# Kernel optimization log

Hardware: AMD Instinct MI355X
Metric: run time of the kernel (lower is better)

The kernel has to match this reference:

```python
import jax, jax.numpy as jnp
import numpy as np

N_NODES = 50000
N_EDGES = 800000
D_IN = 128
HID = [128, 64, 64]
N_CLASSES = 2
N_PROTO = 8
K = N_CLASSES * N_PROTO  # 16 = mlp_input_dim


def setup_inputs() -> dict:
    key = jax.random.key(0)
    ks = jax.random.split(key, 16)
    def lin(k, fi, fo):
        kw, kb = jax.random.split(k)
        s = 1.0 / np.sqrt(fi)
        return (jax.random.uniform(kw, (fi, fo), jnp.float32, -s, s),
                jax.random.uniform(kb, (fo,), jnp.float32, -s, s))
    W1, b1 = lin(ks[0], D_IN, HID[0])
    W2, b2 = lin(ks[1], HID[0], HID[1])
    W3, b3 = lin(ks[2], HID[1], HID[2])
    Wf0, bf0 = lin(ks[3], K, K // 2)
    Wf1, bf1 = lin(ks[4], K // 2, 1)
    return {
        'x': jax.random.normal(ks[5], (N_NODES, D_IN), jnp.float32),
        'edge_index': jax.random.randint(ks[6], (2, N_EDGES), 0, N_NODES, jnp.int64),
        'y': jax.random.randint(ks[7], (N_NODES,), 0, 2, jnp.int64),
        'W1': W1, 'b1': b1, 'W2': W2, 'b2': b2, 'W3': W3, 'b3': b3,
        'prototypes': jax.random.normal(ks[8], (N_CLASSES, N_PROTO, HID[2]), jnp.float32),
        'Wf0': Wf0, 'bf0': bf0, 'Wf1': Wf1, 'bf1': bf1,
    }


def reference(x, edge_index, y, W1, b1, W2, b2, W3, b3, prototypes, Wf0, bf0, Wf1, bf1):
    n = x.shape[0]
    loop = jnp.arange(n, dtype=edge_index.dtype)
    src = jnp.concatenate([edge_index[0], loop])  # A + I self loops (GCNConv default)
    dst = jnp.concatenate([edge_index[1], loop])
    deg = jax.ops.segment_sum(jnp.ones(src.shape[0], x.dtype), dst, num_segments=n)
    dinv = jax.lax.rsqrt(deg)  # deg >= 1 thanks to self loops
    enorm = dinv[src] * dinv[dst]  # sym-normalized edge weights

    def gcn(h, W, b):
        msg = (h @ W)[src] * enorm[:, None]  # gather + transform
        return jax.ops.segment_sum(msg, dst, num_segments=n) + b  # scatter-add

    h = jax.nn.relu(gcn(x, W1, b1))
    h = jax.nn.relu(gcn(h, W2, b2))
    h = jax.nn.relu(gcn(h, W3, b3))  # [n, 64]

    prot = prototypes.reshape(-1, prototypes.shape[-1])  # [K, 64]
    d2 = jnp.maximum(jnp.sum(h * h, -1, keepdims=True)
                     + jnp.sum(prot * prot, -1)[None, :]
                     - 2.0 * (h @ prot.T), 0.0)  # squared Euclidean [n, K]
    sim = jnp.log((d2 + 1.0) / (d2 + 1e-4))

    # MLPReadout, eval mode (dropout inactive), exact GELU like torch nn.GELU
    z = jax.nn.gelu(sim @ Wf0 + bf0, approximate=False)
    out = jax.nn.sigmoid(z @ Wf1 + bf1)
    return (out.squeeze(), y.astype(jnp.float32))
```

## Files before the change

kernel.cpp:

```cpp
#include <hip/hip_runtime.h>
#include <hip/hip_bf16.h>
#include <math.h>


typedef __attribute__((ext_vector_type(8))) short short8;
typedef __attribute__((ext_vector_type(4))) float f32x4;

#define BKT_SHIFT 5
#define BKT_NODES 32
#define EPB 2048
#define LCAP 1024
#define PREPN 28672
#define PREPB 112

__device__ __forceinline__ short f2bs(float x) {
    __hip_bfloat16 b = __float2bfloat16(x);
    return *reinterpret_cast<short*>(&b);
}
__device__ __forceinline__ float2 bpair(unsigned u) {
    float lo = __uint_as_float(u << 16);
    float hi = __uint_as_float(u & 0xffff0000u);
    return make_float2(lo, hi);
}
__device__ __forceinline__ unsigned packbf(float a, float b) {
    unsigned la = (unsigned)(unsigned short)f2bs(a);
    unsigned hb = (unsigned)(unsigned short)f2bs(b);
    return la | (hb << 16);
}

__device__ __forceinline__ void block_excl_scan(int* __restrict__ arr, int n, int t) {
    __shared__ int wsums[4];
    int lane = t & 63, wv = t >> 6;
    int carry = 0;
    for (int c0 = 0; c0 < n; c0 += 256) {
        int i = c0 + t;
        int v = (i < n) ? arr[i] : 0;
        int orig = v;
#pragma unroll
        for (int off = 1; off < 64; off <<= 1) {
            int u = __shfl_up(v, off, 64);
            if (lane >= off) v += u;
        }
        if (lane == 63) wsums[wv] = v;
        __syncthreads();
        int w0 = wsums[0], w1 = wsums[1], w2 = wsums[2], w3 = wsums[3];
        int woff = (wv > 0 ? w0 : 0) + (wv > 1 ? w1 : 0) + (wv > 2 ? w2 : 0);
        int tot = w0 + w1 + w2 + w3;
        __syncthreads();
        if (i < n) arr[i] = carry + woff + (v - orig);
        carry += tot;
    }
}


__global__ __launch_bounds__(256) void sort_local_kernel(const int* __restrict__ ei, int E,
                                                         int NB, int B,
                                                         int* __restrict__ glens,
                                                         int* __restrict__ gstart,
                                                         int* __restrict__ edge_sorted,
                                                         const float* __restrict__ W1,
                                                         const float* __restrict__ W2,
                                                         const float* __restrict__ W3,
                                                         __hip_bfloat16* __restrict__ Wp1,
                                                         __hip_bfloat16* __restrict__ Wp2,
                                                         __hip_bfloat16* __restrict__ Wp3) {
    int t = threadIdx.x;
    if ((int)blockIdx.x >= B) {
        int i = ((int)blockIdx.x - B) * 256 + t;
        if (i < 16384) {
            int k = i >> 7, n = i & 127;
            Wp1[(((k >> 3) * 128) + n) * 8 + (k & 7)] = __float2bfloat16(W1[i]);
        } else if (i < 24576) {
            int j = i - 16384;
            int k = j >> 6, n = j & 63;
            Wp2[(((k >> 3) * 64) + n) * 8 + (k & 7)] = __float2bfloat16(W2[j]);
        } else if (i < PREPN) {
            int j = i - 24576;
            int k = j >> 6, n = j & 63;
            Wp3[(((k >> 3) * 64) + n) * 8 + (k & 7)] = __float2bfloat16(W3[j]);
        }
        return;
    }
    extern __shared__ int lds[];
    int* hist  = lds;
    int* lbase = lds + NB;
    int* sortd = lds + 2 * NB;
    int blk = blockIdx.x;
    int e0 = blk * EPB;
    int cnt = E - e0;
    if (cnt > EPB) cnt = EPB;

    for (int i = t; i < NB; i += 256) hist[i] = 0;
    __syncthreads();
    for (int i = t; i < cnt; i += 256) {
        int dst = ei[E + e0 + i];
        atomicAdd(&hist[dst >> BKT_SHIFT], 1);
    }
    __syncthreads();
    for (int i = t; i < NB; i += 256) lbase[i] = hist[i];
    __syncthreads();
    block_excl_scan(lbase, NB, t);
    __syncthreads();
    for (int i = t; i < NB; i += 256) {
        glens[(size_t)blk * NB + i] = hist[i];
        gstart[(size_t)blk * NB + i] = lbase[i];
    }
    __syncthreads();
    for (int i = t; i < cnt; i += 256) {
        int src = ei[e0 + i];
        int dst = ei[E + e0 + i];
        int pos = atomicAdd(&lbase[dst >> BKT_SHIFT], 1);
        sortd[pos] = (src << BKT_SHIFT) | (dst & (BKT_NODES - 1));
    }
    __syncthreads();
    for (int i = t; i < cnt; i += 256) edge_sorted[e0 + i] = sortd[i];
}

__global__ __launch_bounds__(256) void csr_build_kernel(const int* __restrict__ edge_sorted,
                                                        const int* __restrict__ glens,
                                                        const int* __restrict__ gstart,
                                                        int NB, int B, int N,
                                                        int* __restrict__ row_beg,
                                                        int* __restrict__ row_end,
                                                        float* __restrict__ dinv,
                                                        int* __restrict__ csr) {
    __shared__ int lruns[512];
    __shared__ int loffs[512];
    __shared__ int sdeg[BKT_NODES];
    __shared__ int scur[BKT_NODES];
    __shared__ int raw[LCAP];
    __shared__ int srt[LCAP];
    int b = blockIdx.x;
    int t = threadIdx.x;

    for (int i = t; i < 512; i += 256) {
        int v = (i < B) ? glens[(size_t)i * NB + b] : 0;
        lruns[i] = v;
        loffs[i] = v;
    }
    if (t < BKT_NODES) sdeg[t] = 0;
    __syncthreads();
    block_excl_scan(loffs, B, t);
    __syncthreads();
    int cnt = loffs[B - 1] + lruns[B - 1];
    if (cnt > LCAP) cnt = LCAP;

    for (int r = t; r < B; r += 256) {
        int len = lruns[r];
        if (len) {
            int off = loffs[r];
            int st = r * EPB + gstart[(size_t)r * NB + b];
            for (int k = 0; k < len; ++k) {
                int p = off + k;
                if (p < LCAP) raw[p] = edge_sorted[st + k];
            }
        }
    }
    __syncthreads();

    for (int i = t; i < cnt; i += 256) atomicAdd(&sdeg[raw[i] & (BKT_NODES - 1)], 1);
    __syncthreads();
    int base = b * LCAP;
    if (t < BKT_NODES) {
        int ssum = 0;
        for (int i = 0; i < t; ++i) ssum += sdeg[i];
        scur[t] = ssum;
        int node = b * BKT_NODES + t;
        if (node < N) {
            row_beg[node] = base + ssum;
            row_end[node] = base + ssum + sdeg[t];
            dinv[node] = rsqrtf((float)(sdeg[t] + 1));
        }
    }
    __syncthreads();
    for (int i = t; i < cnt; i += 256) {
        int p = raw[i];
        int pos = atomicAdd(&scur[p & (BKT_NODES - 1)], 1);
        srt[pos] = p >> BKT_SHIFT;
    }
    __syncthreads();
    for (int i = t; i < cnt; i += 256) csr[base + i] = srt[i];
}


template <int DI, int DO, bool AF32>
__global__ __launch_bounds__(256) void mfma_gemm_kernel(const void* __restrict__ Av,
                                                        const __hip_bfloat16* __restrict__ Wp,
                                                        const float* __restrict__ dinv,
                                                        __hip_bfloat16* __restrict__ C, int N) {
    constexpr int NT = DO / 16;
    int t = threadIdx.x;
    int wave = t >> 6, lane = t & 63;
    int q = lane >> 4, l16 = lane & 15;
    int rbase = blockIdx.x * 64 + wave * 16;
    int row = rbase + l16;
    int rowc = row < N ? row : N - 1;

    f32x4 acc[NT];
#pragma unroll
    for (int i = 0; i < NT; ++i) acc[i] = (f32x4){0.f, 0.f, 0.f, 0.f};

#pragma unroll
    for (int kt = 0; kt < DI / 32; ++kt) {
        int k0 = kt * 32 + q * 8;
        short8 afrag;
        if (AF32) {
            const float* A = (const float*)Av;
            const float* ap = A + (size_t)rowc * DI + k0;
            float4 lo = *(const float4*)ap;
            float4 hi = *(const float4*)(ap + 4);
            afrag[0] = f2bs(lo.x); afrag[1] = f2bs(lo.y);
            afrag[2] = f2bs(lo.z); afrag[3] = f2bs(lo.w);
            afrag[4] = f2bs(hi.x); afrag[5] = f2bs(hi.y);
            afrag[6] = f2bs(hi.z); afrag[7] = f2bs(hi.w);
        } else {
            const __hip_bfloat16* A = (const __hip_bfloat16*)Av;
            afrag = *(const short8*)(A + (size_t)rowc * DI + k0);
        }
        const short8* wrow = (const short8*)(Wp + (size_t)(kt * 4 + q) * DO * 8);
#pragma unroll
        for (int tt = 0; tt < NT; ++tt) {
            short8 bfrag = wrow[tt * 16 + l16];
            acc[tt] = __builtin_amdgcn_mfma_f32_16x16x32_bf16(afrag, bfrag, acc[tt], 0, 0, 0);
        }
    }
#pragma unroll
    for (int r = 0; r < 4; ++r) {
        int gr = rbase + q * 4 + r;
        if (gr < N) {
            float dv = dinv[gr];
#pragma unroll
            for (int tt = 0; tt < NT; ++tt)
                C[(size_t)gr * DO + tt * 16 + l16] = __float2bfloat16(acc[tt][r] * dv);
        }
    }
}


__global__ __launch_bounds__(256) void agg128_kernel(const uint4* __restrict__ tmp,
                                                     const float* __restrict__ bias,
                                                     const float* __restrict__ dinv,
                                                     const int* __restrict__ row_beg,
                                                     const int* __restrict__ row_end,
                                                     const int* __restrict__ csr_src,
                                                     uint4* __restrict__ outp, int N) {
    int lane = threadIdx.x & 63;
    int q = lane >> 4, sub = lane & 15;
    int node = blockIdx.x * 4 + (threadIdx.x >> 6);
    if (node >= N) return;
    float dvi = dinv[node];
    float a0 = 0, a1 = 0, a2 = 0, a3 = 0, a4 = 0, a5 = 0, a6 = 0, a7 = 0;
    if (q == 0) {
        uint4 sv = tmp[(size_t)node * 16 + sub];
        float2 p0 = bpair(sv.x), p1 = bpair(sv.y), p2 = bpair(sv.z), p3 = bpair(sv.w);
        a0 = p0.x; a1 = p0.y; a2 = p1.x; a3 = p1.y;
        a4 = p2.x; a5 = p2.y; a6 = p3.x; a7 = p3.y;
    }
    int beg = row_beg[node], end = row_end[node];
    for (int j = beg; j < end; j += 64) {
        int m = end - j;
        if (m > 64) m = 64;
        int s = (lane < m) ? csr_src[j + lane] : 0;
        int iters = (m + 3) >> 2;
        for (int k = 0; k < iters; ++k) {
            int e = 4 * k + q;
            int ec = (e < m) ? e : 0;
            int sk = __shfl(s, ec, 64);
            uint4 v = tmp[(size_t)sk * 16 + sub];
            if (e < m) {
                float2 p0 = bpair(v.x), p1 = bpair(v.y), p2 = bpair(v.z), p3 = bpair(v.w);
                a0 += p0.x; a1 += p0.y; a2 += p1.x; a3 += p1.y;
                a4 += p2.x; a5 += p2.y; a6 += p3.x; a7 += p3.y;
            }
        }
    }
    a0 += __shfl_xor(a0, 16, 64); a1 += __shfl_xor(a1, 16, 64);
    a2 += __shfl_xor(a2, 16, 64); a3 += __shfl_xor(a3, 16, 64);
    a4 += __shfl_xor(a4, 16, 64); a5 += __shfl_xor(a5, 16, 64);
    a6 += __shfl_xor(a6, 16, 64); a7 += __shfl_xor(a7, 16, 64);
    a0 += __shfl_xor(a0, 32, 64); a1 += __shfl_xor(a1, 32, 64);
    a2 += __shfl_xor(a2, 32, 64); a3 += __shfl_xor(a3, 32, 64);
    a4 += __shfl_xor(a4, 32, 64); a5 += __shfl_xor(a5, 32, 64);
    a6 += __shfl_xor(a6, 32, 64); a7 += __shfl_xor(a7, 32, 64);
    if (q == 0) {
        float4 b0 = *(const float4*)&bias[sub * 8];
        float4 b1 = *(const float4*)&bias[sub * 8 + 4];
        uint4 o;
        o.x = packbf(fmaxf(dvi * a0 + b0.x, 0.f), fmaxf(dvi * a1 + b0.y, 0.f));
        o.y = packbf(fmaxf(dvi * a2 + b0.z, 0.f), fmaxf(dvi * a3 + b0.w, 0.f));
        o.z = packbf(fmaxf(dvi * a4 + b1.x, 0.f), fmaxf(dvi * a5 + b1.y, 0.f));
        o.w = packbf(fmaxf(dvi * a6 + b1.z, 0.f), fmaxf(dvi * a7 + b1.w, 0.f));
        outp[(size_t)node * 16 + sub] = o;
    }
}

__global__ __launch_bounds__(256) void agg64_kernel(const uint4* __restrict__ tmp,
                                                    const float* __restrict__ bias,
                                                    const float* __restrict__ dinv,
                                                    const int* __restrict__ row_beg,
                                                    const int* __restrict__ row_end,
                                                    const int* __restrict__ csr_src,
                                                    uint4* __restrict__ outp, int N) {
    int lane = threadIdx.x & 63;
    int o8 = lane >> 3, sub = lane & 7;
    int node = blockIdx.x * 4 + (threadIdx.x >> 6);
    if (node >= N) return;
    float dvi = dinv[node];
    float a0 = 0, a1 = 0, a2 = 0, a3 = 0, a4 = 0, a5 = 0, a6 = 0, a7 = 0;
    if (o8 == 0) {
        uint4 sv = tmp[(size_t)node * 8 + sub];
        float2 p0 = bpair(sv.x), p1 = bpair(sv.y), p2 = bpair(sv.z), p3 = bpair(sv.w);
        a0 = p0.x; a1 = p0.y; a2 = p1.x; a3 = p1.y;
        a4 = p2.x; a5 = p2.y; a6 = p3.x; a7 = p3.y;
    }
    int beg = row_beg[node], end = row_end[node];
    for (int j = beg; j < end; j += 64) {
        int m = end - j;
        if (m > 64) m = 64;
        int s = (lane < m) ? csr_src[j + lane] : 0;
        int iters = (m + 7) >> 3;
        for (int k = 0; k < iters; ++k) {
            int e = 8 * k + o8;
            int ec = (e < m) ? e : 0;
            int sk = __shfl(s, ec, 64);
            uint4 v = tmp[(size_t)sk * 8 + sub];
            if (e < m) {
                float2 p0 = bpair(v.x), p1 = bpair(v.y), p2 = bpair(v.z), p3 = bpair(v.w);
                a0 += p0.x; a1 += p0.y; a2 += p1.x; a3 += p1.y;
                a4 += p2.x; a5 += p2.y; a6 += p3.x; a7 += p3.y;
            }
        }
    }
    a0 += __shfl_xor(a0, 8, 64); a1 += __shfl_xor(a1, 8, 64);
    a2 += __shfl_xor(a2, 8, 64); a3 += __shfl_xor(a3, 8, 64);
    a4 += __shfl_xor(a4, 8, 64); a5 += __shfl_xor(a5, 8, 64);
    a6 += __shfl_xor(a6, 8, 64); a7 += __shfl_xor(a7, 8, 64);
    a0 += __shfl_xor(a0, 16, 64); a1 += __shfl_xor(a1, 16, 64);
    a2 += __shfl_xor(a2, 16, 64); a3 += __shfl_xor(a3, 16, 64);
    a4 += __shfl_xor(a4, 16, 64); a5 += __shfl_xor(a5, 16, 64);
    a6 += __shfl_xor(a6, 16, 64); a7 += __shfl_xor(a7, 16, 64);
    a0 += __shfl_xor(a0, 32, 64); a1 += __shfl_xor(a1, 32, 64);
    a2 += __shfl_xor(a2, 32, 64); a3 += __shfl_xor(a3, 32, 64);
    a4 += __shfl_xor(a4, 32, 64); a5 += __shfl_xor(a5, 32, 64);
    a6 += __shfl_xor(a6, 32, 64); a7 += __shfl_xor(a7, 32, 64);
    if (o8 == 0) {
        float4 b0 = *(const float4*)&bias[sub * 8];
        float4 b1 = *(const float4*)&bias[sub * 8 + 4];
        uint4 o;
        o.x = packbf(fmaxf(dvi * a0 + b0.x, 0.f), fmaxf(dvi * a1 + b0.y, 0.f));
        o.y = packbf(fmaxf(dvi * a2 + b0.z, 0.f), fmaxf(dvi * a3 + b0.w, 0.f));
        o.z = packbf(fmaxf(dvi * a4 + b1.x, 0.f), fmaxf(dvi * a5 + b1.y, 0.f));
        o.w = packbf(fmaxf(dvi * a6 + b1.z, 0.f), fmaxf(dvi * a7 + b1.w, 0.f));
        outp[(size_t)node * 8 + sub] = o;
    }
}


__global__ __launch_bounds__(256) void head_kernel(const unsigned* __restrict__ h,
                                                   const float* __restrict__ protos,
                                                   const float* __restrict__ Wf0,
                                                   const float* __restrict__ bf0,
                                                   const float* __restrict__ Wf1,
                                                   const float* __restrict__ bf1,
                                                   const int* __restrict__ y,
                                                   float* __restrict__ out, int N) {
    __shared__ float Hl[64 * 65];
    __shared__ float Pl[16 * 65];
    __shared__ float hh[64];
    __shared__ float pp[16];
    __shared__ float sim[64 * 17];
    __shared__ float Wf0l[128];
    __shared__ float bf0l[8];
    __shared__ float Wf1l[8];
    __shared__ float bf1l;
    int t = threadIdx.x;
    int n0 = blockIdx.x * 64;

    for (int idx = t; idx < 64 * 32; idx += 256) {
        int r = idx >> 5, c = idx & 31;
        int g = n0 + r;
        unsigned u = (g < N) ? h[(size_t)g * 32 + c] : 0u;
        float2 v = bpair(u);
        Hl[r * 65 + 2 * c] = v.x;
        Hl[r * 65 + 2 * c + 1] = v.y;
    }
    for (int idx = t; idx < 16 * 64; idx += 256) {
        int r = idx >> 6, c = idx & 63;
        Pl[r * 65 + c] = protos[idx];
    }
    if (t < 128) Wf0l[t] = Wf0[t];
    if (t < 8) { bf0l[t] = bf0[t]; Wf1l[t] = Wf1[t]; }
    if (t == 0) bf1l = bf1[0];
    __syncthreads();

    if (t < 64) {
        float s = 0.0f;
        for (int k = 0; k < 64; ++k) { float v = Hl[t * 65 + k]; s += v * v; }
        hh[t] = s;
    } else if (t < 80) {
        int p = t - 64;
        float s = 0.0f;
        for (int k = 0; k < 64; ++k) { float v = Pl[p * 65 + k]; s += v * v; }
        pp[p] = s;
    }
    __syncthreads();

    {
        int node = t & 63;
        int p4 = (t >> 6) * 4;
        float d0 = 0, d1 = 0, d2 = 0, d3 = 0;
        for (int k = 0; k < 64; ++k) {
            float hv = Hl[node * 65 + k];
            d0 += hv * Pl[(p4 + 0) * 65 + k];
            d1 += hv * Pl[(p4 + 1) * 65 + k];
            d2 += hv * Pl[(p4 + 2) * 65 + k];
            d3 += hv * Pl[(p4 + 3) * 65 + k];
        }
        float hhv = hh[node];
        float dd[4] = {d0, d1, d2, d3};
#pragma unroll
        for (int j = 0; j < 4; ++j) {
            float q = hhv + pp[p4 + j] - 2.0f * dd[j];
            q = q > 0.0f ? q : 0.0f;
            sim[node * 17 + p4 + j] = logf((q + 1.0f) / (q + 1e-4f));
        }
    }
    __syncthreads();

    if (t < 64) {
        int g = n0 + t;
        if (g < N) {
            float zacc = bf1l;
#pragma unroll
            for (int o = 0; o < 8; ++o) {
                float s = bf0l[o];
#pragma unroll
                for (int i2 = 0; i2 < 16; ++i2) s += sim[t * 17 + i2] * Wf0l[i2 * 8 + o];
                float gz = 0.5f * s * (1.0f + erff(s * 0.70710678118654752f));
                zacc += gz * Wf1l[o];
            }
            out[g] = 1.0f / (1.0f + expf(-zacc));
        }
    } else if (t < 128) {
        int g = n0 + (t - 64);
        if (g < N) out[N + g] = (float)y[g];
    }
}


extern "C" void kernel_launch(void* const* d_in, const int* in_sizes, int n_in,
                              void* d_out, int out_size, void* d_ws, size_t ws_size,
                              hipStream_t stream) {
    const float* x   = (const float*)d_in[0];
    const int*   ei  = (const int*)d_in[1];
    const int*   y   = (const int*)d_in[2];
    const float* W1  = (const float*)d_in[3];
    const float* b1  = (const float*)d_in[4];
    const float* W2  = (const float*)d_in[5];
    const float* b2  = (const float*)d_in[6];
    const float* W3  = (const float*)d_in[7];
    const float* b3  = (const float*)d_in[8];
    const float* pr  = (const float*)d_in[9];
    const float* Wf0 = (const float*)d_in[10];
    const float* bf0 = (const float*)d_in[11];
    const float* Wf1 = (const float*)d_in[12];
    const float* bf1 = (const float*)d_in[13];
    float* outp = (float*)d_out;

    const int N = in_sizes[2];
    const int E = in_sizes[1] / 2;
    const int NB = (N + BKT_NODES - 1) / BKT_NODES;
    const int B = (E + EPB - 1) / EPB;

    char* w = (char*)d_ws;
    auto carve = [&](size_t bytes) {
        char* p = w;
        w += (bytes + 511) & ~(size_t)511;
        return p;
    };
    int*   glens   = (int*)carve((size_t)B * NB * 4);
    int*   gstart  = (int*)carve((size_t)B * NB * 4);
    int*   esort   = (int*)carve((size_t)B * EPB * 4);
    int*   row_beg = (int*)carve((size_t)N * 4);
    int*   row_end = (int*)carve((size_t)N * 4);
    float* dinv    = (float*)carve((size_t)N * 4);
    int*   csr     = (int*)carve((size_t)NB * LCAP * 4);
    __hip_bfloat16* Wp1 = (__hip_bfloat16*)carve(16384 * 2);
    __hip_bfloat16* Wp2 = (__hip_bfloat16*)carve(8192 * 2);
    __hip_bfloat16* Wp3 = (__hip_bfloat16*)carve(4096 * 2);
    __hip_bfloat16* bufT = (__hip_bfloat16*)carve((size_t)N * 128 * 2);
    __hip_bfloat16* bufH = (__hip_bfloat16*)carve((size_t)N * 128 * 2);

    size_t sort_lds = (size_t)(2 * NB + EPB) * 4;

    sort_local_kernel<<<B + PREPB, 256, sort_lds, stream>>>(ei, E, NB, B, glens, gstart, esort,
                                                            W1, W2, W3, Wp1, Wp2, Wp3);
    csr_build_kernel<<<NB, 256, 0, stream>>>(esort, glens, gstart, NB, B, N,
                                             row_beg, row_end, dinv, csr);

    mfma_gemm_kernel<128, 128, true><<<(N + 63) / 64, 256, 0, stream>>>(x, Wp1, dinv, bufT, N);
    agg128_kernel<<<(N + 3) / 4, 256, 0, stream>>>((const uint4*)bufT, b1, dinv, row_beg, row_end,
                                                   csr, (uint4*)bufH, N);
    mfma_gemm_kernel<128, 64, false><<<(N + 63) / 64, 256, 0, stream>>>(bufH, Wp2, dinv, bufT, N);
    agg64_kernel<<<(N + 3) / 4, 256, 0, stream>>>((const uint4*)bufT, b2, dinv, row_beg, row_end,
                                                  csr, (uint4*)bufH, N);
    mfma_gemm_kernel<64, 64, false><<<(N + 63) / 64, 256, 0, stream>>>(bufH, Wp3, dinv, bufT, N);
    agg64_kernel<<<(N + 3) / 4, 256, 0, stream>>>((const uint4*)bufT, b3, dinv, row_beg, row_end,
                                                  csr, (uint4*)bufH, N);
    head_kernel<<<(N + 63) / 64, 256, 0, stream>>>((const unsigned*)bufH, pr, Wf0, bf0, Wf1, bf1,
                                                   y, outp, N);
}
```

Before: 246.1 us.

## Fuse first-layer GEMM into CSR build kernel and move dinv scaling into aggregation

The first-layer GEMM (x @ W1) no longer depends on dinv. It now runs as extra blocks inside the CSR build launch, so the dense transform overlaps the graph preprocessing and one kernel launch is removed. To make this possible, agg128 applies the source-node dinv per edge by loading dinv[src] alongside the CSR index and broadcasting it by shuffle. This adds a gather and a multiply per edge. The mixed launch may also cause load imbalance between the CSR blocks and the GEMM blocks.

```diff
diff --git a/kernel.cpp b/kernel.cpp
--- a/kernel.cpp
+++ b/kernel.cpp
@@ -116,14 +116,58 @@
     for (int i = t; i < cnt; i += 256) edge_sorted[e0 + i] = sortd[i];
 }
 
-__global__ __launch_bounds__(256) void csr_build_kernel(const int* __restrict__ edge_sorted,
+
+__global__ __launch_bounds__(256) void csr_gemm1_kernel(const int* __restrict__ edge_sorted,
                                                         const int* __restrict__ glens,
                                                         const int* __restrict__ gstart,
                                                         int NB, int B, int N,
                                                         int* __restrict__ row_beg,
                                                         int* __restrict__ row_end,
                                                         float* __restrict__ dinv,
-                                                        int* __restrict__ csr) {
+                                                        int* __restrict__ csr,
+                                                        const float* __restrict__ X,
+                                                        const __hip_bfloat16* __restrict__ Wp1,
+                                                        __hip_bfloat16* __restrict__ T1) {
+    int t = threadIdx.x;
+    if ((int)blockIdx.x >= NB) {
+        int bid = (int)blockIdx.x - NB;
+        int wave = t >> 6, lane = t & 63;
+        int q = lane >> 4, l16 = lane & 15;
+        int rbase = bid * 64 + wave * 16;
+        int row = rbase + l16;
+        int rowc = row < N ? row : N - 1;
+        f32x4 acc[8];
+#pragma unroll
+        for (int i = 0; i < 8; ++i) acc[i] = (f32x4){0.f, 0.f, 0.f, 0.f};
+#pragma unroll
+        for (int kt = 0; kt < 4; ++kt) {
+            int k0 = kt * 32 + q * 8;
+            const float* ap = X + (size_t)rowc * 128 + k0;
+            float4 lo = *(const float4*)ap;
+            float4 hi = *(const float4*)(ap + 4);
+            short8 afrag;
+            afrag[0] = f2bs(lo.x); afrag[1] = f2bs(lo.y);
+            afrag[2] = f2bs(lo.z); afrag[3] = f2bs(lo.w);
+            afrag[4] = f2bs(hi.x); afrag[5] = f2bs(hi.y);
+            afrag[6] = f2bs(hi.z); afrag[7] = f2bs(hi.w);
+            const short8* wrow = (const short8*)(Wp1 + (size_t)(kt * 4 + q) * 128 * 8);
+#pragma unroll
+            for (int tt = 0; tt < 8; ++tt) {
+                short8 bfrag = wrow[tt * 16 + l16];
+                acc[tt] = __builtin_amdgcn_mfma_f32_16x16x32_bf16(afrag, bfrag, acc[tt], 0, 0, 0);
+            }
+        }
+#pragma unroll
+        for (int r = 0; r < 4; ++r) {
+            int gr = rbase + q * 4 + r;
+            if (gr < N) {
+#pragma unroll
+                for (int tt = 0; tt < 8; ++tt)
+                    T1[(size_t)gr * 128 + tt * 16 + l16] = __float2bfloat16(acc[tt][r]);
+            }
+        }
+        return;
+    }
     __shared__ int lruns[512];
     __shared__ int loffs[512];
     __shared__ int sdeg[BKT_NODES];
@@ -131,7 +175,6 @@
     __shared__ int raw[LCAP];
     __shared__ int srt[LCAP];
     int b = blockIdx.x;
-    int t = threadIdx.x;
 
     for (int i = t; i < 512; i += 256) {
         int v = (i < B) ? glens[(size_t)i * NB + b] : 0;
@@ -157,7 +200,6 @@
         }
     }
     __syncthreads();
-
     for (int i = t; i < cnt; i += 256) atomicAdd(&sdeg[raw[i] & (BKT_NODES - 1)], 1);
     __syncthreads();
     int base = b * LCAP;
@@ -183,8 +225,8 @@
 }
 
 
-template <int DI, int DO, bool AF32>
-__global__ __launch_bounds__(256) void mfma_gemm_kernel(const void* __restrict__ Av,
+template <int DI, int DO>
+__global__ __launch_bounds__(256) void mfma_gemm_kernel(const __hip_bfloat16* __restrict__ A,
                                                         const __hip_bfloat16* __restrict__ Wp,
                                                         const float* __restrict__ dinv,
                                                         __hip_bfloat16* __restrict__ C, int N) {
@@ -203,20 +245,7 @@
 #pragma unroll
     for (int kt = 0; kt < DI / 32; ++kt) {
         int k0 = kt * 32 + q * 8;
-        short8 afrag;
-        if (AF32) {
-            const float* A = (const float*)Av;
-            const float* ap = A + (size_t)rowc * DI + k0;
-            float4 lo = *(const float4*)ap;
-            float4 hi = *(const float4*)(ap + 4);
-            afrag[0] = f2bs(lo.x); afrag[1] = f2bs(lo.y);
-            afrag[2] = f2bs(lo.z); afrag[3] = f2bs(lo.w);
-            afrag[4] = f2bs(hi.x); afrag[5] = f2bs(hi.y);
-            afrag[6] = f2bs(hi.z); afrag[7] = f2bs(hi.w);
-        } else {
-            const __hip_bfloat16* A = (const __hip_bfloat16*)Av;
-            afrag = *(const short8*)(A + (size_t)rowc * DI + k0);
-        }
+        short8 afrag = *(const short8*)(A + (size_t)rowc * DI + k0);
         const short8* wrow = (const short8*)(Wp + (size_t)(kt * 4 + q) * DO * 8);
 #pragma unroll
         for (int tt = 0; tt < NT; ++tt) {
@@ -253,24 +282,27 @@
     if (q == 0) {
         uint4 sv = tmp[(size_t)node * 16 + sub];
         float2 p0 = bpair(sv.x), p1 = bpair(sv.y), p2 = bpair(sv.z), p3 = bpair(sv.w);
-        a0 = p0.x; a1 = p0.y; a2 = p1.x; a3 = p1.y;
-        a4 = p2.x; a5 = p2.y; a6 = p3.x; a7 = p3.y;
+        a0 = dvi * p0.x; a1 = dvi * p0.y; a2 = dvi * p1.x; a3 = dvi * p1.y;
+        a4 = dvi * p2.x; a5 = dvi * p2.y; a6 = dvi * p3.x; a7 = dvi * p3.y;
     }
     int beg = row_beg[node], end = row_end[node];
     for (int j = beg; j < end; j += 64) {
         int m = end - j;
         if (m > 64) m = 64;
-        int s = (lane < m) ? csr_src[j + lane] : 0;
+        int s = 0;
+        float dv = 0.0f;
+        if (lane < m) { s = csr_src[j + lane]; dv = dinv[s]; }
         int iters = (m + 3) >> 2;
         for (int k = 0; k < iters; ++k) {
             int e = 4 * k + q;
             int ec = (e < m) ? e : 0;
             int sk = __shfl(s, ec, 64);
+            float dk = __shfl(dv, ec, 64);
             uint4 v = tmp[(size_t)sk * 16 + sub];
             if (e < m) {
                 float2 p0 = bpair(v.x), p1 = bpair(v.y), p2 = bpair(v.z), p3 = bpair(v.w);
-                a0 += p0.x; a1 += p0.y; a2 += p1.x; a3 += p1.y;
-                a4 += p2.x; a5 += p2.y; a6 += p3.x; a7 += p3.y;
+                a0 += dk * p0.x; a1 += dk * p0.y; a2 += dk * p1.x; a3 += dk * p1.y;
+                a4 += dk * p2.x; a5 += dk * p2.y; a6 += dk * p3.x; a7 += dk * p3.y;
             }
         }
     }
@@ -331,18 +363,13 @@
             }
         }
     }
-    a0 += __shfl_xor(a0, 8, 64); a1 += __shfl_xor(a1, 8, 64);
-    a2 += __shfl_xor(a2, 8, 64); a3 += __shfl_xor(a3, 8, 64);
-    a4 += __shfl_xor(a4, 8, 64); a5 += __shfl_xor(a5, 8, 64);
-    a6 += __shfl_xor(a6, 8, 64); a7 += __shfl_xor(a7, 8, 64);
-    a0 += __shfl_xor(a0, 16, 64); a1 += __shfl_xor(a1, 16, 64);
-    a2 += __shfl_xor(a2, 16, 64); a3 += __shfl_xor(a3, 16, 64);
-    a4 += __shfl_xor(a4, 16, 64); a5 += __shfl_xor(a5, 16, 64);
-    a6 += __shfl_xor(a6, 16, 64); a7 += __shfl_xor(a7, 16, 64);
-    a0 += __shfl_xor(a0, 32, 64); a1 += __shfl_xor(a1, 32, 64);
-    a2 += __shfl_xor(a2, 32, 64); a3 += __shfl_xor(a3, 32, 64);
-    a4 += __shfl_xor(a4, 32, 64); a5 += __shfl_xor(a5, 32, 64);
-    a6 += __shfl_xor(a6, 32, 64); a7 += __shfl_xor(a7, 32, 64);
+#pragma unroll
+    for (int off = 8; off <= 32; off <<= 1) {
+        a0 += __shfl_xor(a0, off, 64); a1 += __shfl_xor(a1, off, 64);
+        a2 += __shfl_xor(a2, off, 64); a3 += __shfl_xor(a3, off, 64);
+        a4 += __shfl_xor(a4, off, 64); a5 += __shfl_xor(a5, off, 64);
+        a6 += __shfl_xor(a6, off, 64); a7 += __shfl_xor(a7, off, 64);
+    }
     if (o8 == 0) {
         float4 b0 = *(const float4*)&bias[sub * 8];
         float4 b1 = *(const float4*)&bias[sub * 8 + 4];
@@ -492,21 +519,22 @@
     __hip_bfloat16* bufH = (__hip_bfloat16*)carve((size_t)N * 128 * 2);
 
     size_t sort_lds = (size_t)(2 * NB + EPB) * 4;
+    const int gemm1_blocks = (N + 63) / 64;
+    const int agg_blocks = (N + 3) / 4;
 
     sort_local_kernel<<<B + PREPB, 256, sort_lds, stream>>>(ei, E, NB, B, glens, gstart, esort,
                                                             W1, W2, W3, Wp1, Wp2, Wp3);
-    csr_build_kernel<<<NB, 256, 0, stream>>>(esort, glens, gstart, NB, B, N,
-                                             row_beg, row_end, dinv, csr);
-
-    mfma_gemm_kernel<128, 128, true><<<(N + 63) / 64, 256, 0, stream>>>(x, Wp1, dinv, bufT, N);
-    agg128_kernel<<<(N + 3) / 4, 256, 0, stream>>>((const uint4*)bufT, b1, dinv, row_beg, row_end,
-                                                   csr, (uint4*)bufH, N);
-    mfma_gemm_kernel<128, 64, false><<<(N + 63) / 64, 256, 0, stream>>>(bufH, Wp2, dinv, bufT, N);
-    agg64_kernel<<<(N + 3) / 4, 256, 0, stream>>>((const uint4*)bufT, b2, dinv, row_beg, row_end,
+    csr_gemm1_kernel<<<NB + gemm1_blocks, 256, 0, stream>>>(esort, glens, gstart, NB, B, N,
+                                                            row_beg, row_end, dinv, csr,
+                                                            x, Wp1, bufT);
+    agg128_kernel<<<agg_blocks, 256, 0, stream>>>((const uint4*)bufT, b1, dinv, row_beg, row_end,
                                                   csr, (uint4*)bufH, N);
-    mfma_gemm_kernel<64, 64, false><<<(N + 63) / 64, 256, 0, stream>>>(bufH, Wp3, dinv, bufT, N);
-    agg64_kernel<<<(N + 3) / 4, 256, 0, stream>>>((const uint4*)bufT, b3, dinv, row_beg, row_end,
-                                                  csr, (uint4*)bufH, N);
+    mfma_gemm_kernel<128, 64><<<gemm1_blocks, 256, 0, stream>>>(bufH, Wp2, dinv, bufT, N);
+    agg64_kernel<<<agg_blocks, 256, 0, stream>>>((const uint4*)bufT, b2, dinv, row_beg, row_end,
+                                                 csr, (uint4*)bufH, N);
+    mfma_gemm_kernel<64, 64><<<gemm1_blocks, 256, 0, stream>>>(bufH, Wp3, dinv, bufT, N);
+    agg64_kernel<<<agg_blocks, 256, 0, stream>>>((const uint4*)bufT, b3, dinv, row_beg, row_end,
+                                                 csr, (uint4*)bufH, N);
     head_kernel<<<(N + 63) / 64, 256, 0, stream>>>((const unsigned*)bufH, pr, Wf0, bf0, Wf1, bf1,
                                                    y, outp, N);
 }
```

After: 245.4 us. Within noise of the previous version (-0.3%).
